# Performance work log

Measured on AMD Instinct MI355X. Metric: run time of the kernel, lower is better.

The kernel has to match this reference:

```python
import jax, jax.numpy as jnp
import numpy as np
from jax import lax

EPS = 1e-5      # InstanceNorm2d default eps
SLOPE = 0.2     # LeakyReLU negative slope
K = 3           # kernel size
PAD = 1


def _conv(x, w, pad=PAD):
    # x: [B,C,H,W], w: [O,I,K,K], stride 1
    return lax.conv_general_dilated(x, w, (1, 1), [(pad, pad), (pad, pad)],
                                    dimension_numbers=('NCHW', 'OIHW', 'NCHW'))


def _instance_norm(x, gamma, beta):
    mu = jnp.mean(x, (2, 3), keepdims=True)
    var = jnp.mean((x - mu) ** 2, (2, 3), keepdims=True)
    xn = (x - mu) * lax.rsqrt(var + EPS)
    return xn * gamma[None, :, None, None] + beta[None, :, None, None]


def _lrelu(x):
    return jnp.where(x >= 0, x, SLOPE * x)


def _deform_conv(x, w_off, b_off, w_def):
    # DCNv2: offsets+mask predicted by a 3x3 conv, then modulated bilinear sampling.
    B, C, H, W = x.shape
    om = _conv(x, w_off) + b_off[None, :, None, None]       # [B, 3*K*K, H, W]
    o1, o2, m = jnp.split(om, 3, axis=1)                    # each [B, K*K, H, W]
    off = jnp.concatenate([o1, o2], axis=1)                 # [B, 2*K*K, H, W]
    dy = off[:, 0::2]                                       # [B, K*K, H, W] y-offsets
    dx = off[:, 1::2]                                       # [B, K*K, H, W] x-offsets
    mask = jax.nn.sigmoid(m)                                # [B, K*K, H, W]

    ky = jnp.repeat(jnp.arange(K), K).astype(x.dtype)       # tap row index per k
    kx = jnp.tile(jnp.arange(K), K).astype(x.dtype)         # tap col index per k
    py = dy + jnp.arange(H, dtype=x.dtype)[None, None, :, None] - PAD + ky[None, :, None, None]
    px = dx + jnp.arange(W, dtype=x.dtype)[None, None, None, :] - PAD + kx[None, :, None, None]

    y0 = jnp.floor(py); x0 = jnp.floor(px)
    ly = py - y0; lx = px - x0
    y0i = y0.astype(jnp.int32); x0i = x0.astype(jnp.int32)

    xf = x.reshape(B, C, H * W)

    def gather(iy, ix):
        valid = ((iy >= 0) & (iy < H) & (ix >= 0) & (ix < W)).astype(x.dtype)
        idx = jnp.clip(iy, 0, H - 1) * W + jnp.clip(ix, 0, W - 1)
        v = jax.vmap(lambda f, i: jnp.take(f, i, axis=-1))(xf, idx)  # [B,C,K*K,H,W]
        return v * valid[:, None]

    samp = (gather(y0i, x0i)         * ((1 - ly) * (1 - lx))[:, None]
          + gather(y0i, x0i + 1)     * ((1 - ly) * lx)[:, None]
          + gather(y0i + 1, x0i)     * (ly * (1 - lx))[:, None]
          + gather(y0i + 1, x0i + 1) * (ly * lx)[:, None])          # [B,C,K*K,H,W]

    wk = w_def.reshape(w_def.shape[0], C, K * K)            # [O,C,K*K]
    return jnp.einsum('ock,bckhw,bkhw->bohw', wk, samp, mask)


def setup_inputs() -> dict:
    key = jax.random.key(0)
    ks = jax.random.split(key, 10)
    B, C, H, W = 4, 128, 96, 96
    x = jax.random.normal(ks[0], (B, C, H, W), jnp.float32)
    g1 = 1.0 + 0.05 * jax.random.normal(ks[1], (C,), jnp.float32)
    b1 = 0.05 * jax.random.normal(ks[2], (C,), jnp.float32)
    g2 = 1.0 + 0.05 * jax.random.normal(ks[3], (C,), jnp.float32)
    b2 = 0.05 * jax.random.normal(ks[4], (C,), jnp.float32)
    w1 = jax.random.normal(ks[5], (C, C, K, K), jnp.float32) * 0.03
    bc1 = 0.01 * jax.random.normal(ks[6], (C,), jnp.float32)
    # offset/mask conv: zero-init in the original; use small random values so the
    # irregular bilinear-sampling path is actually exercised.
    w_off = jax.random.normal(ks[7], (3 * K * K, C, K, K), jnp.float32) * 0.01
    b_off = 0.01 * jax.random.normal(ks[8], (3 * K * K,), jnp.float32)
    w_def = jax.random.normal(ks[9], (C, C, K, K), jnp.float32) * 0.03  # DeformConv has bias=None
    return {"x": x, "g1": g1, "b1": b1, "g2": g2, "b2": b2,
            "w1": w1, "bc1": bc1, "w_off": w_off, "b_off": b_off, "w_def": w_def}


def reference(x, g1, b1, g2, b2, w1, bc1, w_off, b_off, w_def):
    h = _lrelu(_instance_norm(x, g1, b1))
    h = _conv(h, w1) + bc1[None, :, None, None]
    h = _lrelu(_instance_norm(h, g2, b2))
    h = _deform_conv(h, w_off, b_off, w_def)
    return h + x
```

## Files before the change

kernel.cpp:

```cpp
#include <hip/hip_runtime.h>
#include <hip/hip_fp16.h>
#include <math.h>

#define HWN 9216
#define HD 96
#define WD 96

typedef _Float16 h8v __attribute__((ext_vector_type(8)));
typedef float f16x16 __attribute__((ext_vector_type(16)));

__device__ __forceinline__ ushort f2h(float f) {
  return __half_as_ushort(__float2half(f));
}
__device__ __forceinline__ __half2 u2h(unsigned u) {
  return __builtin_bit_cast(__half2, u);
}
__device__ __forceinline__ unsigned h2u(__half2 h) {
  return __builtin_bit_cast(unsigned, h);
}
__device__ __forceinline__ h8v u4h(uint4 v) {
  return __builtin_bit_cast(h8v, v);
}
__device__ __forceinline__ f16x16 mfma32(h8v a, h8v b, f16x16 c) {
  return __builtin_amdgcn_mfma_f32_32x32x16_f16(a, b, c, 0, 0, 0);
}
__device__ __forceinline__ __half2 pkmax2(__half2 a, __half2 b) {
  unsigned r;
  asm("v_pk_max_f16 %0, %1, %2" : "=v"(r) : "v"(h2u(a)), "v"(h2u(b)));
  return u2h(r);
}
__device__ __forceinline__ __half2 lrelu2(__half2 v, __half2 c02) {
  return pkmax2(v, __hmul2(v, c02));
}

__global__ __launch_bounds__(256) void packxt_kernel(
    const float* __restrict__ w1, const float* __restrict__ wdef,
    const float* __restrict__ woff, const float* __restrict__ x,
    ushort* __restrict__ w1p, ushort* __restrict__ wdp, ushort* __restrict__ wofp,
    unsigned* __restrict__ xh, float* __restrict__ partS, float* __restrict__ partQ) {
  __shared__ float tl[128][97];
  int bid = blockIdx.x;
  int t = threadIdx.x;
  if (bid < 162) {
    int i = bid * 256 + t;
    const float* src;
    ushort* dst;
    int CT, CO_real, fi;
    if (i < 18432) { src = w1; dst = w1p; CT = 4; CO_real = 128; fi = i; }
    else if (i < 36864) { src = wdef; dst = wdp; CT = 4; CO_real = 128; fi = i - 18432; }
    else { src = woff; dst = wofp; CT = 1; CO_real = 27; fi = i - 36864; }
    int lane = fi & 63;
    int j = fi >> 6;
    int ks = j & 7; j >>= 3;
    int ct = j % CT;
    int kk = j / CT;
    int co = ct * 32 + (lane & 31);
    int c0 = ks * 16 + (lane >> 5) * 8;
    ushort fr[8];
#pragma unroll
    for (int e = 0; e < 8; ++e) {
      float v = 0.f;
      if (co < CO_real) v = src[(size_t)(co * 128 + c0 + e) * 9 + kk];
      fr[e] = f2h(v);
    }
    uint4 o4;
    o4.x = (unsigned)fr[0] | ((unsigned)fr[1] << 16);
    o4.y = (unsigned)fr[2] | ((unsigned)fr[3] << 16);
    o4.z = (unsigned)fr[4] | ((unsigned)fr[5] << 16);
    o4.w = (unsigned)fr[6] | ((unsigned)fr[7] << 16);
    *(uint4*)(dst + (size_t)fi * 8) = o4;
    return;
  }
  int xb = bid - 162;
  int b = xb / 96, y = xb % 96;
  const float* sbase = x + (size_t)b * 128 * HWN + y * WD;
  for (int i = t; i < 12288; i += 256) {
    int c = i / 96, xx = i - c * 96;
    tl[c][xx] = sbase[(size_t)c * HWN + xx];
  }
  __syncthreads();
  {
    int c = t >> 1, half = t & 1;
    float S = 0.f, Q = 0.f;
    for (int j = 0; j < 48; ++j) {
      float v = tl[c][half * 48 + j];
      S += v;
      Q += v * v;
    }
    S += __shfl_xor(S, 1, 64);
    Q += __shfl_xor(Q, 1, 64);
    if (half == 0) {
      partS[((size_t)(b * 96 + y)) * 128 + c] = S;
      partQ[((size_t)(b * 96 + y)) * 128 + c] = Q;
    }
  }
  unsigned* dbase = xh + (size_t)(b * 96 + y) * 96 * 64;
  for (int i = t; i < 6144; i += 256) {
    int xx = i >> 6, c2 = i & 63;
    unsigned lo = f2h(tl[2 * c2][xx]);
    unsigned hi = f2h(tl[2 * c2 + 1][xx]);
    dbase[xx * 64 + c2] = lo | (hi << 16);
  }
}

__global__ __launch_bounds__(64) void finalize_kernel(
    const float* __restrict__ partS, const float* __restrict__ partQ,
    const float* __restrict__ gamma, const float* __restrict__ beta,
    float* __restrict__ sa_, float* __restrict__ sb_, int ntiles) {
  int bc = blockIdx.x;
  int b = bc >> 7, c = bc & 127;
  float S = 0.f, Q = 0.f;
  for (int tl = threadIdx.x; tl < ntiles; tl += 64) {
    S += partS[((size_t)b * ntiles + tl) * 128 + c];
    Q += partQ[((size_t)b * ntiles + tl) * 128 + c];
  }
#pragma unroll
  for (int off = 32; off > 0; off >>= 1) {
    S += __shfl_down(S, off, 64);
    Q += __shfl_down(Q, off, 64);
  }
  if (threadIdx.x == 0) {
    float mu = S / (float)HWN;
    float var = Q / (float)HWN - mu * mu;
    float rs = rsqrtf(var + 1e-5f);
    float a = rs * gamma[c];
    sa_[bc] = a;
    sb_[bc] = beta[c] - mu * a;
  }
}

__global__ __launch_bounds__(512) void conv1_mfma(
    const ushort* __restrict__ inp, const float* __restrict__ sa_,
    const float* __restrict__ sb_, const ushort* __restrict__ wp,
    const float* __restrict__ bias, ushort* __restrict__ outh,
    float* __restrict__ partS, float* __restrict__ partQ) {
  __shared__ ushort halo[100 * 128];
  __shared__ __half2 sah[64], sbh[64];
  int b = blockIdx.y;
  int tile = blockIdx.x;
  int Y0 = (tile / 12) * 8, X0 = (tile % 12) * 8;
  int t = threadIdx.x;
  int lane = t & 63, w = t >> 6;
  if (t < 64) {
    sah[t] = __floats2half2_rn(sa_[b * 128 + 2 * t], sa_[b * 128 + 2 * t + 1]);
    sbh[t] = __floats2half2_rn(sb_[b * 128 + 2 * t], sb_[b * 128 + 2 * t + 1]);
  }
  __syncthreads();
  const __half2 c02 = __float2half2_rn(0.2f);
  const ushort* ib = inp + (size_t)b * HWN * 128;
  for (int i = t; i < 400; i += 512) {
    int r = i >> 2, q = i & 3;
    int gy = Y0 - 1 + r / 10, gx = X0 - 1 + r % 10;
    bool inb = ((unsigned)gy < 96u) && ((unsigned)gx < 96u);
    const uint4* gp4 = (const uint4*)(ib + (size_t)(gy * 96 + gx) * 128 + q * 32);
#pragma unroll
    for (int cc = 0; cc < 4; ++cc) {
      uint4 v = make_uint4(0, 0, 0, 0);
      if (inb) {
        uint4 g = gp4[cc];
        unsigned ar[4] = {g.x, g.y, g.z, g.w};
        int c2b = (q * 4 + cc) * 4;
#pragma unroll
        for (int j = 0; j < 4; ++j) {
          __half2 hv = __hfma2(u2h(ar[j]), sah[c2b + j], sbh[c2b + j]);
          hv = lrelu2(hv, c02);
          ar[j] = h2u(hv);
        }
        v.x = ar[0]; v.y = ar[1]; v.z = ar[2]; v.w = ar[3];
      }
      int ch = (q * 4 + cc) ^ (r & 7);
      *(uint4*)&halo[r * 128 + ch * 8] = v;
    }
  }
  __syncthreads();

  int ct = w >> 1, pt = w & 1;
  int pl = lane & 31, kh = lane >> 5;
  int p = pt * 32 + pl;
  f16x16 acc = (f16x16)(0.f);

  uint4 Acur[8], Anxt[8];
#pragma unroll
  for (int ks = 0; ks < 8; ++ks)
    Acur[ks] = *(const uint4*)(wp + (size_t)((0 * 4 + ct) * 8 + ks) * 512 + lane * 8);

  for (int kk = 0; kk < 9; ++kk) {
    if (kk < 8) {
#pragma unroll
      for (int ks = 0; ks < 8; ++ks)
        Anxt[ks] = *(const uint4*)(wp + (size_t)(((kk + 1) * 4 + ct) * 8 + ks) * 512 + lane * 8);
    }
    int ky = kk / 3, kx = kk % 3;
    int r = ((p >> 3) + ky) * 10 + (p & 7) + kx;
    __builtin_amdgcn_s_setprio(1);
#pragma unroll
    for (int ks = 0; ks < 8; ++ks) {
      int u = (ks * 2 + kh) ^ (r & 7);
      h8v bf = *(const h8v*)&halo[r * 128 + u * 8];
      acc = mfma32(u4h(Acur[ks]), bf, acc);
    }
    __builtin_amdgcn_s_setprio(0);
    if (kk < 8) {
#pragma unroll
      for (int ks = 0; ks < 8; ++ks) Acur[ks] = Anxt[ks];
    }
  }
  int gp = (Y0 + (p >> 3)) * 96 + X0 + (p & 7);
  float s[16], q[16];
#pragma unroll
  for (int g = 0; g < 4; ++g) {
    int ch0 = ct * 32 + 4 * kh + 8 * g;
    float v0 = acc[4 * g + 0] + bias[ch0 + 0];
    float v1 = acc[4 * g + 1] + bias[ch0 + 1];
    float v2 = acc[4 * g + 2] + bias[ch0 + 2];
    float v3 = acc[4 * g + 3] + bias[ch0 + 3];
    uint2 o;
    o.x = (unsigned)f2h(v0) | ((unsigned)f2h(v1) << 16);
    o.y = (unsigned)f2h(v2) | ((unsigned)f2h(v3) << 16);
    *(uint2*)&outh[((size_t)b * HWN + gp) * 128 + ch0] = o;
    s[4 * g + 0] = v0; s[4 * g + 1] = v1; s[4 * g + 2] = v2; s[4 * g + 3] = v3;
    q[4 * g + 0] = v0 * v0; q[4 * g + 1] = v1 * v1;
    q[4 * g + 2] = v2 * v2; q[4 * g + 3] = v3 * v3;
  }
#pragma unroll
  for (int r = 0; r < 16; ++r)
#pragma unroll
    for (int m = 1; m < 32; m <<= 1) {
      s[r] += __shfl_xor(s[r], m, 64);
      q[r] += __shfl_xor(q[r], m, 64);
    }
  if (pl == 0) {
    size_t base = ((size_t)b * 288 + tile * 2 + pt) * 128;
#pragma unroll
    for (int r = 0; r < 16; ++r) {
      int co = ct * 32 + 4 * kh + (r & 3) + 8 * (r >> 2);
      partS[base + co] = s[r];
      partQ[base + co] = q[r];
    }
  }
}

__device__ __forceinline__ uint4 gaffine(const ushort* hb, int pix, int cc,
                                         const __half2* sa2v, const __half2* sb2v,
                                         __half2 c02) {
  uint4 g = *(const uint4*)(hb + (size_t)pix * 128 + cc * 8);
  unsigned ar[4] = {g.x, g.y, g.z, g.w};
#pragma unroll
  for (int j = 0; j < 4; ++j) {
    __half2 hv = __hfma2(u2h(ar[j]), sa2v[j], sb2v[j]);
    hv = lrelu2(hv, c02);
    ar[j] = h2u(hv);
  }
  return make_uint4(ar[0], ar[1], ar[2], ar[3]);
}

__global__ __launch_bounds__(512) void deform_fused(
    const ushort* __restrict__ h2n, const float* __restrict__ sa_,
    const float* __restrict__ sb_, const ushort* __restrict__ wofp,
    const float* __restrict__ boff, const ushort* __restrict__ wdp,
    const float* __restrict__ x, float* __restrict__ out) {
  __shared__ __align__(16) ushort halo[144 * 128];
  __shared__ __align__(16) ushort S[64 * 128];
  __shared__ __align__(16) ushort4 idxs[9][64];
  __shared__ __align__(16) unsigned wgtb[9][64][4];
  __shared__ float om_t[32][64];
  __shared__ __half2 sah[64], sbh[64];
  int bid = blockIdx.x;
  int swz = (bid & 7) * 72 + (bid >> 3);
  int b = swz / 144;
  int tile = swz % 144;
  int Y0 = (tile / 12) * 8, X0 = (tile % 12) * 8;
  int t = threadIdx.x;
  int lane = t & 63, w = t >> 6;
  const ushort* hb = h2n + (size_t)b * HWN * 128;
  if (t < 64) {
    sah[t] = __floats2half2_rn(sa_[b * 128 + 2 * t], sa_[b * 128 + 2 * t + 1]);
    sbh[t] = __floats2half2_rn(sb_[b * 128 + 2 * t], sb_[b * 128 + 2 * t + 1]);
  }
  __syncthreads();
  const __half2 c02 = __float2half2_rn(0.2f);

  for (int i = t; i < 2304; i += 512) {
    int pix = i >> 4, u = i & 15;
    int gy = Y0 - 2 + pix / 12, gx = X0 - 2 + pix % 12;
    uint4 v = make_uint4(0, 0, 0, 0);
    if (((unsigned)gy < 96u) && ((unsigned)gx < 96u)) {
      uint4 g = *(const uint4*)(hb + (size_t)(gy * 96 + gx) * 128 + u * 8);
      unsigned ar[4] = {g.x, g.y, g.z, g.w};
#pragma unroll
      for (int j = 0; j < 4; ++j) {
        __half2 hv = __hfma2(u2h(ar[j]), sah[u * 4 + j], sbh[u * 4 + j]);
        hv = lrelu2(hv, c02);
        ar[j] = h2u(hv);
      }
      v.x = ar[0]; v.y = ar[1]; v.z = ar[2]; v.w = ar[3];
    }
    *(uint4*)&halo[pix * 128 + ((u ^ (pix & 15)) * 8)] = v;
  }
  __syncthreads();

  if (w < 2) {
    int pt = w;
    int pl = lane & 31, kh = lane >> 5;
    int p = pt * 32 + pl;
    f16x16 accm = (f16x16)(0.f);
    uint4 Ac[8], An[8];
#pragma unroll
    for (int ks = 0; ks < 8; ++ks)
      Ac[ks] = *(const uint4*)(wofp + (size_t)(0 * 8 + ks) * 512 + lane * 8);
    for (int kk = 0; kk < 9; ++kk) {
      if (kk < 8) {
#pragma unroll
        for (int ks = 0; ks < 8; ++ks)
          An[ks] = *(const uint4*)(wofp + (size_t)((kk + 1) * 8 + ks) * 512 + lane * 8);
      }
      int ky = kk / 3, kx = kk % 3;
      int hp = (1 + (p >> 3) + ky) * 12 + 1 + (p & 7) + kx;
      __builtin_amdgcn_s_setprio(1);
#pragma unroll
      for (int ks = 0; ks < 8; ++ks) {
        int u = (ks * 2 + kh) ^ (hp & 15);
        h8v bf = *(const h8v*)&halo[hp * 128 + u * 8];
        accm = mfma32(u4h(Ac[ks]), bf, accm);
      }
      __builtin_amdgcn_s_setprio(0);
      if (kk < 8) {
#pragma unroll
        for (int ks = 0; ks < 8; ++ks) Ac[ks] = An[ks];
      }
    }
#pragma unroll
    for (int reg = 0; reg < 16; ++reg) {
      int co = 4 * kh + (reg & 3) + 8 * (reg >> 2);
      if (co < 27) om_t[co][p] = accm[reg] + boff[co];
    }
  }
  __syncthreads();

  for (int i = t; i < 576; i += 512) {
    int k = i >> 6, p = i & 63;
    int yy = Y0 + (p >> 3), xx = X0 + (p & 7);
    float dy = om_t[2 * k][p];
    float dx = om_t[2 * k + 1][p];
    float mv = om_t[18 + k][p];
    float mask = 1.0f / (1.0f + expf(-mv));
    float py = dy + (float)(yy - 1 + (k / 3));
    float px = dx + (float)(xx - 1 + (k % 3));
    float fy = floorf(py), fx = floorf(px);
    float lyf = py - fy, lxf = px - fx;
    int y0 = (int)fy, x0 = (int)fx;
    int y1 = y0 + 1, x1 = x0 + 1;
    bool vy0 = (y0 >= 0) && (y0 < HD);
    bool vy1 = (y1 >= 0) && (y1 < HD);
    bool vx0 = (x0 >= 0) && (x0 < WD);
    bool vx1 = (x1 >= 0) && (x1 < WD);
    int y0c = min(max(y0, 0), HD - 1), y1c = min(max(y1, 0), HD - 1);
    int x0c = min(max(x0, 0), WD - 1), x1c = min(max(x1, 0), WD - 1);
    float w0 = (1.f - lyf) * (1.f - lxf) * ((vy0 && vx0) ? mask : 0.f);
    float w1v = (1.f - lyf) * lxf * ((vy0 && vx1) ? mask : 0.f);
    float w2 = lyf * (1.f - lxf) * ((vy1 && vx0) ? mask : 0.f);
    float w3 = lyf * lxf * ((vy1 && vx1) ? mask : 0.f);
    bool inh = (y0c >= Y0 - 2) && (y1c <= Y0 + 9) && (x0c >= X0 - 2) && (x1c <= X0 + 9);
    ushort4 sidx;
    if (inh) {
      int sy0 = y0c - (Y0 - 2), sy1 = y1c - (Y0 - 2);
      int sx0 = x0c - (X0 - 2), sx1 = x1c - (X0 - 2);
      sidx.x = (ushort)(sy0 * 12 + sx0);
      sidx.y = (ushort)(sy0 * 12 + sx1);
      sidx.z = (ushort)(sy1 * 12 + sx0);
      sidx.w = (ushort)(sy1 * 12 + sx1);
    } else {
      sidx.x = (ushort)((y0c * WD + x0c) | 0x8000);
      sidx.y = (ushort)(y0c * WD + x1c);
      sidx.z = (ushort)(y1c * WD + x0c);
      sidx.w = (ushort)(y1c * WD + x1c);
    }
    idxs[k][p] = sidx;
    wgtb[k][p][0] = (unsigned)f2h(w0) * 0x10001u;
    wgtb[k][p][1] = (unsigned)f2h(w1v) * 0x10001u;
    wgtb[k][p][2] = (unsigned)f2h(w2) * 0x10001u;
    wgtb[k][p][3] = (unsigned)f2h(w3) * 0x10001u;
  }
  __syncthreads();

  int cc = t & 15;
  int pp = t >> 4;
  int ct = w >> 1, pt = w & 1;
  int pl = lane & 31, kh = lane >> 5;
  int pg = pt * 32 + pl;
  f16x16 acc = (f16x16)(0.f);
  __half2 sa2v[4], sb2v[4];
#pragma unroll
  for (int j = 0; j < 4; ++j) { sa2v[j] = sah[cc * 4 + j]; sb2v[j] = sbh[cc * 4 + j]; }

  uint4 AW[8];
  for (int k = 0; k < 9; ++k) {
    const ushort* wk = wdp + (size_t)k * 16384;
#pragma unroll
    for (int ks = 0; ks < 8; ++ks)
      AW[ks] = *(const uint4*)(wk + (size_t)(ct * 8 + ks) * 512 + lane * 8);
#pragma unroll
    for (int i2 = 0; i2 < 2; ++i2) {
      int p = pp + 32 * i2;
      ushort4 sidx = idxs[k][p];
      uint4 wb = *(const uint4*)&wgtb[k][p][0];
      uint4 C0, C1, C2, C3;
      if (sidx.x & 0x8000u) {
        C0 = gaffine(hb, sidx.x & 0x7fff, cc, sa2v, sb2v, c02);
        C1 = gaffine(hb, sidx.y, cc, sa2v, sb2v, c02);
        C2 = gaffine(hb, sidx.z, cc, sa2v, sb2v, c02);
        C3 = gaffine(hb, sidx.w, cc, sa2v, sb2v, c02);
      } else {
        C0 = *(const uint4*)&halo[sidx.x * 128 + ((cc ^ (sidx.x & 15)) * 8)];
        C1 = *(const uint4*)&halo[sidx.y * 128 + ((cc ^ (sidx.y & 15)) * 8)];
        C2 = *(const uint4*)&halo[sidx.z * 128 + ((cc ^ (sidx.z & 15)) * 8)];
        C3 = *(const uint4*)&halo[sidx.w * 128 + ((cc ^ (sidx.w & 15)) * 8)];
      }
      __half2 a0 = u2h(wb.x), a1 = u2h(wb.y), a2 = u2h(wb.z), a3 = u2h(wb.w);
      __half2 s0 = __hmul2(u2h(C0.x), a0);
      __half2 s1 = __hmul2(u2h(C0.y), a0);
      __half2 s2 = __hmul2(u2h(C0.z), a0);
      __half2 s3 = __hmul2(u2h(C0.w), a0);
      s0 = __hfma2(u2h(C1.x), a1, s0); s1 = __hfma2(u2h(C1.y), a1, s1);
      s2 = __hfma2(u2h(C1.z), a1, s2); s3 = __hfma2(u2h(C1.w), a1, s3);
      s0 = __hfma2(u2h(C2.x), a2, s0); s1 = __hfma2(u2h(C2.y), a2, s1);
      s2 = __hfma2(u2h(C2.z), a2, s2); s3 = __hfma2(u2h(C2.w), a2, s3);
      s0 = __hfma2(u2h(C3.x), a3, s0); s1 = __hfma2(u2h(C3.y), a3, s1);
      s2 = __hfma2(u2h(C3.z), a3, s2); s3 = __hfma2(u2h(C3.w), a3, s3);
      uint4 o4;
      o4.x = h2u(s0); o4.y = h2u(s1); o4.z = h2u(s2); o4.w = h2u(s3);
      *(uint4*)&S[p * 128 + ((cc ^ (p & 15)) * 8)] = o4;
    }
    asm volatile("s_waitcnt lgkmcnt(0)" ::: "memory");
    __builtin_amdgcn_s_barrier();
    __builtin_amdgcn_s_setprio(1);
#pragma unroll
    for (int ks = 0; ks < 8; ++ks) {
      int u = (ks * 2 + kh) ^ (pg & 15);
      h8v bf = *(const h8v*)&S[pg * 128 + u * 8];
      acc = mfma32(u4h(AW[ks]), bf, acc);
    }
    __builtin_amdgcn_s_setprio(0);
    asm volatile("s_waitcnt lgkmcnt(0)" ::: "memory");
    __builtin_amdgcn_s_barrier();
  }
  int gp = (Y0 + (pg >> 3)) * 96 + X0 + (pg & 7);
#pragma unroll
  for (int reg = 0; reg < 16; ++reg) {
    int co = ct * 32 + 4 * kh + (reg & 3) + 8 * (reg >> 2);
    size_t oi = (size_t)(b * 128 + co) * HWN + gp;
    out[oi] = acc[reg] + x[oi];
  }
}

extern "C" void kernel_launch(void* const* d_in, const int* in_sizes, int n_in,
                              void* d_out, int out_size, void* d_ws, size_t ws_size,
                              hipStream_t stream) {
  const float* x = (const float*)d_in[0];
  const float* g1 = (const float*)d_in[1];
  const float* b1 = (const float*)d_in[2];
  const float* g2 = (const float*)d_in[3];
  const float* b2 = (const float*)d_in[4];
  const float* w1 = (const float*)d_in[5];
  const float* bc1 = (const float*)d_in[6];
  const float* w_off = (const float*)d_in[7];
  const float* b_off = (const float*)d_in[8];
  const float* w_def = (const float*)d_in[9];
  float* out = (float*)d_out;
  float* ws = (float*)d_ws;

  ushort* w1p = (ushort*)ws;
  ushort* wofp = (ushort*)(ws + 73728);
  ushort* wdp = (ushort*)(ws + 92160);
  float* sa1 = ws + 165888;
  float* sb1 = ws + 166400;
  float* sa2 = ws + 166912;
  float* sb2 = ws + 167424;
  float* partS1 = ws + 167936;
  float* partQ1 = ws + 217088;
  float* partS2 = ws + 266240;
  float* partQ2 = ws + 413696;
  ushort* xh = (ushort*)(ws + 561152);
  ushort* hBh = (ushort*)(ws + 2920448);

  packxt_kernel<<<546, 256, 0, stream>>>(w1, w_def, w_off, x, w1p, wdp, wofp,
                                         (unsigned*)xh, partS1, partQ1);
  finalize_kernel<<<512, 64, 0, stream>>>(partS1, partQ1, g1, b1, sa1, sb1, 96);
  conv1_mfma<<<dim3(144, 4), 512, 0, stream>>>(xh, sa1, sb1, w1p, bc1, hBh, partS2, partQ2);
  finalize_kernel<<<512, 64, 0, stream>>>(partS2, partQ2, g2, b2, sa2, sb2, 288);
  deform_fused<<<dim3(576), 512, 0, stream>>>(hBh, sa2, sb2, wofp, b_off, wdp, x, out);
}
```

Before: 93.99 us.

## Shrink deform tile to 8x4 pixels with 256-thread blocks and compact LDS

The fused deformable-conv kernel now processes 32-pixel tiles (4 rows by 8 columns) per block with 256 threads instead of 64-pixel tiles with 512 threads, doubling the grid to 1152 blocks. Shared memory shrinks because the halo, staging buffer and index arrays are smaller, om_t is aliased onto the staging buffer, and the per-tap bilinear weights are stored as packed ushort4 and broadcast to half2 at use. The goal is more resident blocks per CU and better load balance. In exchange, the halo-to-tile ratio grows, so more halo pixels are loaded and transformed per output. The offset conv runs on one wave instead of two, the deform weight matrix is reloaded by twice as many blocks, and setprio hints are removed.

```diff
diff --git a/kernel.cpp b/kernel.cpp
--- a/kernel.cpp
+++ b/kernel.cpp
@@ -254,22 +254,22 @@
   return make_uint4(ar[0], ar[1], ar[2], ar[3]);
 }
 
-__global__ __launch_bounds__(512) void deform_fused(
+__global__ __launch_bounds__(256) void deform_fused(
     const ushort* __restrict__ h2n, const float* __restrict__ sa_,
     const float* __restrict__ sb_, const ushort* __restrict__ wofp,
     const float* __restrict__ boff, const ushort* __restrict__ wdp,
     const float* __restrict__ x, float* __restrict__ out) {
-  __shared__ __align__(16) ushort halo[144 * 128];
-  __shared__ __align__(16) ushort S[64 * 128];
-  __shared__ __align__(16) ushort4 idxs[9][64];
-  __shared__ __align__(16) unsigned wgtb[9][64][4];
-  __shared__ float om_t[32][64];
+  __shared__ __align__(16) ushort halo[96 * 128];
+  __shared__ __align__(16) ushort S[32 * 128];
+  __shared__ __align__(16) ushort4 idxs[9][32];
+  __shared__ __align__(16) ushort4 wgtc[9][32];
   __shared__ __half2 sah[64], sbh[64];
+  float* om_t = (float*)S;
   int bid = blockIdx.x;
-  int swz = (bid & 7) * 72 + (bid >> 3);
-  int b = swz / 144;
-  int tile = swz % 144;
-  int Y0 = (tile / 12) * 8, X0 = (tile % 12) * 8;
+  int swz = (bid & 7) * 144 + (bid >> 3);
+  int b = swz / 288;
+  int tile = swz % 288;
+  int Y0 = (tile / 12) * 4, X0 = (tile % 12) * 8;
   int t = threadIdx.x;
   int lane = t & 63, w = t >> 6;
   const ushort* hb = h2n + (size_t)b * HWN * 128;
@@ -280,7 +280,7 @@
   __syncthreads();
   const __half2 c02 = __float2half2_rn(0.2f);
 
-  for (int i = t; i < 2304; i += 512) {
+  for (int i = t; i < 1536; i += 256) {
     int pix = i >> 4, u = i & 15;
     int gy = Y0 - 2 + pix / 12, gx = X0 - 2 + pix % 12;
     uint4 v = make_uint4(0, 0, 0, 0);
@@ -299,10 +299,9 @@
   }
   __syncthreads();
 
-  if (w < 2) {
-    int pt = w;
+  if (w == 0) {
     int pl = lane & 31, kh = lane >> 5;
-    int p = pt * 32 + pl;
+    int p = pl;
     f16x16 accm = (f16x16)(0.f);
     uint4 Ac[8], An[8];
 #pragma unroll
@@ -316,14 +315,12 @@
       }
       int ky = kk / 3, kx = kk % 3;
       int hp = (1 + (p >> 3) + ky) * 12 + 1 + (p & 7) + kx;
-      __builtin_amdgcn_s_setprio(1);
 #pragma unroll
       for (int ks = 0; ks < 8; ++ks) {
         int u = (ks * 2 + kh) ^ (hp & 15);
         h8v bf = *(const h8v*)&halo[hp * 128 + u * 8];
         accm = mfma32(u4h(Ac[ks]), bf, accm);
       }
-      __builtin_amdgcn_s_setprio(0);
       if (kk < 8) {
 #pragma unroll
         for (int ks = 0; ks < 8; ++ks) Ac[ks] = An[ks];
@@ -332,17 +329,17 @@
 #pragma unroll
     for (int reg = 0; reg < 16; ++reg) {
       int co = 4 * kh + (reg & 3) + 8 * (reg >> 2);
-      if (co < 27) om_t[co][p] = accm[reg] + boff[co];
-    }
-  }
-  __syncthreads();
-
-  for (int i = t; i < 576; i += 512) {
-    int k = i >> 6, p = i & 63;
+      if (co < 27) om_t[co * 32 + p] = accm[reg] + boff[co];
+    }
+  }
+  __syncthreads();
+
+  for (int i = t; i < 288; i += 256) {
+    int k = i >> 5, p = i & 31;
     int yy = Y0 + (p >> 3), xx = X0 + (p & 7);
-    float dy = om_t[2 * k][p];
-    float dx = om_t[2 * k + 1][p];
-    float mv = om_t[18 + k][p];
+    float dy = om_t[(2 * k) * 32 + p];
+    float dx = om_t[(2 * k + 1) * 32 + p];
+    float mv = om_t[(18 + k) * 32 + p];
     float mask = 1.0f / (1.0f + expf(-mv));
     float py = dy + (float)(yy - 1 + (k / 3));
     float px = dx + (float)(xx - 1 + (k % 3));
@@ -360,7 +357,7 @@
     float w1v = (1.f - lyf) * lxf * ((vy0 && vx1) ? mask : 0.f);
     float w2 = lyf * (1.f - lxf) * ((vy1 && vx0) ? mask : 0.f);
     float w3 = lyf * lxf * ((vy1 && vx1) ? mask : 0.f);
-    bool inh = (y0c >= Y0 - 2) && (y1c <= Y0 + 9) && (x0c >= X0 - 2) && (x1c <= X0 + 9);
+    bool inh = (y0c >= Y0 - 2) && (y1c <= Y0 + 5) && (x0c >= X0 - 2) && (x1c <= X0 + 9);
     ushort4 sidx;
     if (inh) {
       int sy0 = y0c - (Y0 - 2), sy1 = y1c - (Y0 - 2);
@@ -376,18 +373,17 @@
       sidx.w = (ushort)(y1c * WD + x1c);
     }
     idxs[k][p] = sidx;
-    wgtb[k][p][0] = (unsigned)f2h(w0) * 0x10001u;
-    wgtb[k][p][1] = (unsigned)f2h(w1v) * 0x10001u;
-    wgtb[k][p][2] = (unsigned)f2h(w2) * 0x10001u;
-    wgtb[k][p][3] = (unsigned)f2h(w3) * 0x10001u;
+    ushort4 wc;
+    wc.x = f2h(w0); wc.y = f2h(w1v); wc.z = f2h(w2); wc.w = f2h(w3);
+    wgtc[k][p] = wc;
   }
   __syncthreads();
 
   int cc = t & 15;
   int pp = t >> 4;
-  int ct = w >> 1, pt = w & 1;
+  int ct = w;
   int pl = lane & 31, kh = lane >> 5;
-  int pg = pt * 32 + pl;
+  int pg = pl;
   f16x16 acc = (f16x16)(0.f);
   __half2 sa2v[4], sb2v[4];
 #pragma unroll
@@ -401,9 +397,9 @@
       AW[ks] = *(const uint4*)(wk + (size_t)(ct * 8 + ks) * 512 + lane * 8);
 #pragma unroll
     for (int i2 = 0; i2 < 2; ++i2) {
-      int p = pp + 32 * i2;
+      int p = pp + 16 * i2;
       ushort4 sidx = idxs[k][p];
-      uint4 wb = *(const uint4*)&wgtb[k][p][0];
+      ushort4 wc = wgtc[k][p];
       uint4 C0, C1, C2, C3;
       if (sidx.x & 0x8000u) {
         C0 = gaffine(hb, sidx.x & 0x7fff, cc, sa2v, sb2v, c02);
@@ -416,7 +412,10 @@
         C2 = *(const uint4*)&halo[sidx.z * 128 + ((cc ^ (sidx.z & 15)) * 8)];
         C3 = *(const uint4*)&halo[sidx.w * 128 + ((cc ^ (sidx.w & 15)) * 8)];
       }
-      __half2 a0 = u2h(wb.x), a1 = u2h(wb.y), a2 = u2h(wb.z), a3 = u2h(wb.w);
+      __half2 a0 = u2h((unsigned)wc.x * 0x10001u);
+      __half2 a1 = u2h((unsigned)wc.y * 0x10001u);
+      __half2 a2 = u2h((unsigned)wc.z * 0x10001u);
+      __half2 a3 = u2h((unsigned)wc.w * 0x10001u);
       __half2 s0 = __hmul2(u2h(C0.x), a0);
       __half2 s1 = __hmul2(u2h(C0.y), a0);
       __half2 s2 = __hmul2(u2h(C0.z), a0);
@@ -433,14 +432,12 @@
     }
     asm volatile("s_waitcnt lgkmcnt(0)" ::: "memory");
     __builtin_amdgcn_s_barrier();
-    __builtin_amdgcn_s_setprio(1);
 #pragma unroll
     for (int ks = 0; ks < 8; ++ks) {
       int u = (ks * 2 + kh) ^ (pg & 15);
       h8v bf = *(const h8v*)&S[pg * 128 + u * 8];
       acc = mfma32(u4h(AW[ks]), bf, acc);
     }
-    __builtin_amdgcn_s_setprio(0);
     asm volatile("s_waitcnt lgkmcnt(0)" ::: "memory");
     __builtin_amdgcn_s_barrier();
   }
@@ -488,5 +485,5 @@
   finalize_kernel<<<512, 64, 0, stream>>>(partS1, partQ1, g1, b1, sa1, sb1, 96);
   conv1_mfma<<<dim3(144, 4), 512, 0, stream>>>(xh, sa1, sb1, w1p, bc1, hBh, partS2, partQ2);
   finalize_kernel<<<512, 64, 0, stream>>>(partS2, partQ2, g2, b2, sa2, sb2, 288);
-  deform_fused<<<dim3(576), 512, 0, stream>>>(hBh, sa2, sb2, wofp, b_off, wdp, x, out);
-}
+  deform_fused<<<dim3(1152), 256, 0, stream>>>(hBh, sa2, sb2, wofp, b_off, wdp, x, out);
+}
```

Result: faster. 89.58 us (-4.7%).
